# Kernel optimization log

Measured on AMD Instinct MI355X. Metric: run time of the kernel, lower is better.

The kernel has to match this reference:

```python
import jax, jax.numpy as jnp
import numpy as np
from jax import lax

L = 1024       # sequence length
D = 64         # bond_dim
O = 128        # output_dim
P = 2          # d_phys
B = 4096       # batch
SPLIT = L // 2


def _ident(dl, dr):
    # identity boost added to every physical slice: t[k, p, k] += 1 for k < min(dl, dr)
    m = min(dl, dr)
    base = jnp.zeros((dl, dr), dtype=jnp.float32)
    base = base.at[jnp.arange(m), jnp.arange(m)].set(1.0)
    return base[:, None, :]  # (dl, 1, dr) broadcast over p


def setup_inputs() -> dict:
    key = jax.random.key(0)
    k0, k1, k2, k3, k4, k5 = jax.random.split(key, 6)
    x = jax.random.uniform(k0, (B, L), dtype=jnp.float32)
    left0 = jax.random.normal(k1, (1, P, D), dtype=jnp.float32) * 0.01 + _ident(1, D)
    left_rest = jax.random.normal(k2, (SPLIT - 1, D, P, D), dtype=jnp.float32) * 0.01 + _ident(D, D)[None]
    center = jax.random.normal(k3, (D, D, O), dtype=jnp.float32) / jnp.sqrt(jnp.float32(O))
    right_rest = jax.random.normal(k4, (L - SPLIT - 1, D, P, D), dtype=jnp.float32) * 0.01 + _ident(D, D)[None]
    right_last = jax.random.normal(k5, (D, P, 1), dtype=jnp.float32) * 0.01 + _ident(D, 1)
    return {"x": x, "left0": left0, "left_rest": left_rest, "center": center,
            "right_rest": right_rest, "right_last": right_last}


def _norm_env(env):
    return env / (jnp.linalg.norm(env, axis=1, keepdims=True) + 1e-8)


def reference(x, left0, left_rest, center, right_rest, right_last):
    angle = (jnp.pi / 2.0) * x
    phi = jnp.stack([jnp.cos(angle), jnp.sin(angle)], axis=-1)  # (B, L, P)

    # left sweep: first tensor has trivial left bond (=1)
    left = _norm_env(jnp.einsum('pr,bp->br', left0[0], phi[:, 0]))

    def lstep(env, inp):
        A, p = inp  # A: (D,P,D), p: (B,P)
        return _norm_env(jnp.einsum('bl,lpr,bp->br', env, A, p)), None

    phi_l = jnp.swapaxes(phi[:, 1:SPLIT], 0, 1)  # (SPLIT-1, B, P)
    left, _ = lax.scan(lstep, left, (left_rest, phi_l))

    # right sweep (from last site inward): last tensor has trivial right bond (=1)
    right = _norm_env(jnp.einsum('lp,bp->bl', right_last[:, :, 0], phi[:, L - 1]))

    def rstep(env, inp):
        A, p = inp
        return _norm_env(jnp.einsum('br,lpr,bp->bl', env, A, p)), None

    phi_r = jnp.swapaxes(phi[:, SPLIT:L - 1], 0, 1)[::-1]  # reversed order
    right, _ = lax.scan(rstep, right, (right_rest[::-1], phi_r))

    out = jnp.einsum('bl,br,lro->bo', left, right, center)  # (B, O)
    # F.normalize(p=2, dim=1) with eps=1e-12
    return out / jnp.clip(jnp.linalg.norm(out, axis=1, keepdims=True), 1e-12)
```

## Files before the change

### kernel.cpp

```cpp
#include <hip/hip_runtime.h>

typedef float vf4 __attribute__((ext_vector_type(4)));
typedef int vi4 __attribute__((ext_vector_type(4)));
typedef short short8 __attribute__((ext_vector_type(8)));
typedef unsigned short ushort8 __attribute__((ext_vector_type(8)));

#define LL 1024
#define DD 64
#define OO 128
#define BBATCH 4096
#define NS 511
#define SITE_F 8192

__device__ __forceinline__ void gld_lds16(const float* g, float* l) {
  __builtin_amdgcn_global_load_lds(
      (const __attribute__((address_space(1))) unsigned int*)g,
      (__attribute__((address_space(3))) unsigned int*)l, 16, 0, 0);
}

__device__ __forceinline__ void stage32k_256(float* lds, const float* g, int tid) {
#pragma unroll
  for (int q = 0; q < 8; q++) {
    const int off = (q * 256 + tid) * 4;
    gld_lds16(g + off, lds + off);
  }
}

__global__ __launch_bounds__(256) void prep(const float* __restrict__ lsrc,
                                            const float* __restrict__ rsrc,
                                            unsigned short* __restrict__ Wl,
                                            unsigned short* __restrict__ Wr) {
  __shared__ float S[SITE_F];
  const int site = blockIdx.x;
  const int dir = blockIdx.y;
  const int tid = threadIdx.x;
  const float* src = (dir ? rsrc : lsrc) + (size_t)site * SITE_F;
  unsigned short* dst = dir ? (Wr + (size_t)(NS - 1 - site) * SITE_F)
                            : (Wl + (size_t)site * SITE_F);
#pragma unroll
  for (int m = 0; m < 8; m++)
    *(vf4*)&S[(m * 256 + tid) * 4] = *(const vf4*)&src[(m * 256 + tid) * 4];
  __syncthreads();
#pragma unroll
  for (int q = 0; q < 4; q++) {
    const int slot = q * 256 + tid;
    const int lane = slot & 63, f = slot >> 6;
    const int mt = f >> 2, s = f & 3;
    const int g = lane >> 4, c = lane & 15;
    const int m = 16 * mt + c;
    ushort8 t;
#pragma unroll
    for (int j = 0; j < 8; j++) {
      const int k = 32 * s + 8 * g + j;
      float v;
      if (dir == 0) {
        const int l = k >> 1, p = k & 1;
        v = S[l * 128 + p * 64 + m] - ((m == l) ? 1.f : 0.f);
      } else {
        const int r = k >> 1, p = k & 1;
        v = S[m * 128 + p * 64 + r] - ((m == r) ? 1.f : 0.f);
      }
      const unsigned uu = __builtin_bit_cast(unsigned, v);
      t[j] = (unsigned short)((uu + 0x7FFFu + ((uu >> 16) & 1u)) >> 16);
    }
    *(ushort8*)&dst[(size_t)slot * 8] = t;
  }
}

#define STAGE_GROUP(G, BUF)                                                    \
  {                                                                            \
    _Pragma("unroll")                                                          \
    for (int s4 = 0; s4 < 4; s4++) {                                           \
      int st_ = (G) * 4 + s4;                                                  \
      if (st_ > NS - 1) st_ = NS - 1;                                          \
      const float* Ws_ = Wf + (size_t)st_ * 4096;                              \
      float* d_ = &ring[BUF][s4][0];                                           \
      _Pragma("unroll")                                                        \
      for (int q = 0; q < 8; q++)                                              \
        gld_lds16(Ws_ + q * 512 + tid * 4, d_ + q * 512 + tid * 4);            \
    }                                                                          \
  }

#define BODY(I, BUF, S4)                                                       \
  {                                                                            \
    const float* rb = &ring[BUF][S4][0];                                       \
    vf4 FC[16];                                                                \
    _Pragma("unroll")                                                          \
    for (int q = 0; q < 16; q++)                                               \
      FC[q] = *(const vf4*)&rb[(q * 64 + lane) * 4];                           \
    const int nI = (I) + 1;                                                    \
    float xn = 0.f;                                                            \
    if (nI <= NS - 1) xn = xrow[dir ? (1022 - nI) : (1 + nI)];                 \
    short8 e2[4];                                                              \
    _Pragma("unroll")                                                          \
    for (int s = 0; s < 4; s++) {                                              \
      int pk[4];                                                               \
      _Pragma("unroll")                                                        \
      for (int t = 0; t < 4; t++) {                                            \
        const float f0 = u[s][t] * CS, f1 = u[s][t] * SN;                      \
        int p;                                                                 \
        asm("v_cvt_pk_bf16_f32 %0, %1, %2" : "=v"(p) : "v"(f0), "v"(f1));      \
        pk[t] = p;                                                             \
      }                                                                        \
      e2[s] = __builtin_bit_cast(short8, (vi4){pk[0], pk[1], pk[2], pk[3]});   \
    }                                                                          \
    const float keff = CS + SN;                                                \
    vf4 acc[4];                                                                \
    _Pragma("unroll")                                                          \
    for (int mt = 0; mt < 4; mt++) {                                           \
      vf4 z;                                                                   \
      z[0] = keff * u[mt][0]; z[1] = keff * u[mt][1];                          \
      z[2] = keff * u[mt][2]; z[3] = keff * u[mt][3];                          \
      acc[mt] = z;                                                             \
    }                                                                          \
    _Pragma("unroll")                                                          \
    for (int mt = 0; mt < 4; mt++) {                                           \
      acc[mt] = __builtin_amdgcn_mfma_f32_16x16x32_bf16(                       \
          __builtin_bit_cast(short8, FC[mt * 4 + 0]), e2[0], acc[mt], 0, 0, 0);\
      acc[mt] = __builtin_amdgcn_mfma_f32_16x16x32_bf16(                       \
          __builtin_bit_cast(short8, FC[mt * 4 + 1]), e2[1], acc[mt], 0, 0, 0);\
      acc[mt] = __builtin_amdgcn_mfma_f32_16x16x32_bf16(                       \
          __builtin_bit_cast(short8, FC[mt * 4 + 2]), e2[2], acc[mt], 0, 0, 0);\
      acc[mt] = __builtin_amdgcn_mfma_f32_16x16x32_bf16(                       \
          __builtin_bit_cast(short8, FC[mt * 4 + 3]), e2[3], acc[mt], 0, 0, 0);\
    }                                                                          \
    _Pragma("unroll")                                                          \
    for (int mt = 0; mt < 4; mt++) u[mt] = acc[mt];                            \
    if (nI <= NS - 1) {                                   \
      const float qrev = 0.25f * xn;           \
      float c_, s_;                                                            \
      asm("v_cos_f32 %0, %1" : "=v"(c_) : "v"(qrev));                          \
      asm("v_sin_f32 %0, %1" : "=v"(s_) : "v"(qrev));                          \
      CS = c_;                                                                 \
      SN = s_;                                                                 \
    }                                                                          \
    if (((I) & 7) == 7) {         \
      float nss = 0.f;                                                         \
      _Pragma("unroll")                                                        \
      for (int mt = 0; mt < 4; mt++)                                           \
        _Pragma("unroll")                                                      \
        for (int r = 0; r < 4; r++) nss += u[mt][r] * u[mt][r];                \
      nss += __shfl_xor(nss, 16);                                              \
      nss += __shfl_xor(nss, 32);                                              \
      const int eb = (__float_as_int(nss) >> 23) & 0xFF;                       \
      const float alpha = __int_as_float((127 - ((eb - 127) >> 1)) << 23);     \
      _Pragma("unroll")                                                        \
      for (int mt = 0; mt < 4; mt++)                                           \
        _Pragma("unroll")                                                      \
        for (int r = 0; r < 4; r++) u[mt][r] *= alpha;                         \
    }                                                                          \
  }

__global__ __launch_bounds__(128, 1) void sweep(const float* __restrict__ x,
                                                const float* __restrict__ left0,
                                                const float* __restrict__ right_last,
                                                const unsigned short* __restrict__ Wl,
                                                const unsigned short* __restrict__ Wr,
                                                float* __restrict__ envL,
                                                float* __restrict__ envR) {
  __shared__ float ring[2][4][4096];
  const int bid = blockIdx.x;
  const int xcd = bid & 7;
  const int dir = xcd >> 2;
  const int slot = (xcd & 3) * 32 + (bid >> 3);
  const int tid = threadIdx.x;
  const int wave = tid >> 6;
  const int lane = tid & 63;
  const int g_ = lane >> 4, c = lane & 15;
  const int b = (slot * 2 + wave) * 16 + c;
  const float* xrow = x + (size_t)b * LL;

  const float* Wf = (const float*)(dir ? Wr : Wl);

  vf4 u[4];
  {
    const float x0 = xrow[dir ? (LL - 1) : 0];
    const float qrev = 0.25f * x0;
    float cs, sn;
    asm("v_cos_f32 %0, %1" : "=v"(cs) : "v"(qrev));
    asm("v_sin_f32 %0, %1" : "=v"(sn) : "v"(qrev));
#pragma unroll
    for (int mt = 0; mt < 4; mt++)
#pragma unroll
      for (int r = 0; r < 4; r++) {
        const int n = 16 * mt + 4 * g_ + r;
        const float w0 = dir ? right_last[n * 2] : left0[n];
        const float w1 = dir ? right_last[n * 2 + 1] : left0[64 + n];
        u[mt][r] = cs * w0 + sn * w1;
      }
    float ss = 0.f;
#pragma unroll
    for (int mt = 0; mt < 4; mt++)
#pragma unroll
      for (int r = 0; r < 4; r++) ss += u[mt][r] * u[mt][r];
    ss += __shfl_xor(ss, 16);
    ss += __shfl_xor(ss, 32);
    const float a0 = 1.f / (sqrtf(ss) + 1e-8f);
#pragma unroll
    for (int mt = 0; mt < 4; mt++)
#pragma unroll
      for (int r = 0; r < 4; r++) u[mt][r] *= a0;
  }

  float CS, SN;
  {
    const float q0 = 0.25f * xrow[dir ? 1022 : 1];
    asm("v_cos_f32 %0, %1" : "=v"(CS) : "v"(q0));
    asm("v_sin_f32 %0, %1" : "=v"(SN) : "v"(q0));
  }

  STAGE_GROUP(0, 0)
  __syncthreads();

  for (int g = 0; g < 127; g++) {
    const int buf = g & 1;
    STAGE_GROUP(g + 1, buf ^ 1)
    const int i0 = g * 4;
    BODY(i0 + 0, buf, 0)
    BODY(i0 + 1, buf, 1)
    BODY(i0 + 2, buf, 2)
    BODY(i0 + 3, buf, 3)
    __syncthreads();
  }
  BODY(508, 1, 0)
  BODY(509, 1, 1)
  BODY(510, 1, 2)

  float nss = 0.f;
#pragma unroll
  for (int mt = 0; mt < 4; mt++)
#pragma unroll
    for (int r = 0; r < 4; r++) nss += u[mt][r] * u[mt][r];
  nss += __shfl_xor(nss, 16);
  nss += __shfl_xor(nss, 32);
  const float alpha = 1.f / (sqrtf(nss) + 1e-8f);

  float* eo = (dir ? envR : envL) + (size_t)b * 64;
#pragma unroll
  for (int mt = 0; mt < 4; mt++) {
    vf4 v;
#pragma unroll
    for (int r = 0; r < 4; r++) v[r] = u[mt][r] * alpha;
    *(vf4*)&eo[16 * mt + 4 * g_] = v;
  }
}

__global__ __launch_bounds__(256) void centerk(const float* __restrict__ envL,
                                               const float* __restrict__ envR,
                                               const float* __restrict__ center,
                                               float* __restrict__ Pp) {
  __shared__ float Cs[2][SITE_F];
  __shared__ float LT[64 * 36];
  __shared__ float RT[64 * 36];
  const int bbase = blockIdx.x * 32;
  const int half = blockIdx.y;
  const int tid = threadIdx.x;
  const int och = tid & 31, bch = tid >> 5;
  const int o0 = och * 4, b0 = bch * 4;
#pragma unroll
  for (int m = 0; m < 8; m++) {
    const int idx = m * 256 + tid;
    const int b = idx >> 6, l = idx & 63;
    LT[l * 36 + b] = envL[(bbase + b) * 64 + l];
    RT[l * 36 + b] = envR[(bbase + b) * 64 + l];
  }
  stage32k_256(Cs[0], center + (half * 32) * SITE_F, tid);
  float acc[4][4] = {};
  for (int lh = 0; lh < 32; lh++) {
    __syncthreads();
    const int buf = lh & 1;
    if (lh + 1 < 32) stage32k_256(Cs[buf ^ 1], center + (half * 32 + lh + 1) * SITE_F, tid);
    const vf4 lv = *(const vf4*)&LT[(half * 32 + lh) * 36 + b0];
    const float* C = Cs[buf];
#pragma unroll
    for (int r = 0; r < 64; r++) {
      const vf4 rv = *(const vf4*)&RT[r * 36 + b0];
      const vf4 cv = *(const vf4*)&C[r * 128 + o0];
#pragma unroll
      for (int i2 = 0; i2 < 4; i2++) {
        const float w = lv[i2] * rv[i2];
        acc[i2][0] += w * cv[0];
        acc[i2][1] += w * cv[1];
        acc[i2][2] += w * cv[2];
        acc[i2][3] += w * cv[3];
      }
    }
  }
#pragma unroll
  for (int i2 = 0; i2 < 4; i2++) {
    vf4 v; v[0] = acc[i2][0]; v[1] = acc[i2][1]; v[2] = acc[i2][2]; v[3] = acc[i2][3];
    *(vf4*)&Pp[(size_t)half * BBATCH * 128 + (size_t)(bbase + b0 + i2) * 128 + o0] = v;
  }
}

__global__ __launch_bounds__(256) void combinek(const float* __restrict__ P,
                                                float* __restrict__ out) {
  const float* P0 = P;
  const float* P1 = P + (size_t)BBATCH * 128;
  const int row = blockIdx.x * 8 + (threadIdx.x >> 5);
  const int o0 = (threadIdx.x & 31) * 4;
  vf4 v = *(const vf4*)&P0[(size_t)row * 128 + o0];
  const vf4 v1 = *(const vf4*)&P1[(size_t)row * 128 + o0];
  v += v1;
  float ss = v[0] * v[0] + v[1] * v[1] + v[2] * v[2] + v[3] * v[3];
#pragma unroll
  for (int m = 1; m < 32; m <<= 1) ss += __shfl_xor(ss, m);
  const float inv = 1.f / fmaxf(sqrtf(ss), 1e-12f);
  v *= inv;
  *(vf4*)&out[(size_t)row * 128 + o0] = v;
}

extern "C" void kernel_launch(void* const* d_in, const int* in_sizes, int n_in,
                              void* d_out, int out_size, void* d_ws, size_t ws_size,
                              hipStream_t stream) {
  const float* x = (const float*)d_in[0];
  const float* left0 = (const float*)d_in[1];
  const float* left_rest = (const float*)d_in[2];
  const float* center = (const float*)d_in[3];
  const float* right_rest = (const float*)d_in[4];
  const float* right_last = (const float*)d_in[5];
  float* out = (float*)d_out;

  char* wsb = (char*)d_ws;
  unsigned short* Wl = (unsigned short*)wsb;
  unsigned short* Wr = Wl + (size_t)NS * SITE_F;
  float* envL = (float*)(Wr + (size_t)NS * SITE_F);
  float* envR = envL + (size_t)BBATCH * 64;
  float* Pp = envR + (size_t)BBATCH * 64;

  hipLaunchKernelGGL(prep, dim3(NS, 2), dim3(256), 0, stream,
                     left_rest, right_rest, Wl, Wr);
  hipLaunchKernelGGL(sweep, dim3(256), dim3(128), 0, stream,
                     x, left0, right_last, Wl, Wr, envL, envR);
  hipLaunchKernelGGL(centerk, dim3(BBATCH / 32, 2), dim3(256), 0, stream,
                     envL, envR, center, Pp);
  hipLaunchKernelGGL(combinek, dim3(BBATCH / 8), dim3(256), 0, stream, Pp, out);
}
```

Before: 387.6 us.

## Use bf16 MFMA for center contraction and prefetch sweep fragments across sites

The center contraction now runs on bf16 MFMA instead of scalar FP32 FMAs. A new prep2 kernel reformats the center tensor into MFMA fragment layout, and the sweep also writes a bf16 copy of the right environment. Separately, the sweep loop loads the next site's LDS fragments into registers before the current MFMAs run, and splits each accumulation chain into two independent accumulators to shorten dependency latency. The center output no longer needs the two-half partial sum, which simplifies the combine step. In exchange it adds a kernel launch, raises register pressure in the sweep, and lowers precision in the center product.

```diff
diff --git a/kernel.cpp b/kernel.cpp
--- a/kernel.cpp
+++ b/kernel.cpp
@@ -2,6 +2,7 @@
 
 typedef float vf4 __attribute__((ext_vector_type(4)));
 typedef int vi4 __attribute__((ext_vector_type(4)));
+typedef int vi2 __attribute__((ext_vector_type(2)));
 typedef short short8 __attribute__((ext_vector_type(8)));
 typedef unsigned short ushort8 __attribute__((ext_vector_type(8)));
 
@@ -18,12 +19,9 @@
       (__attribute__((address_space(3))) unsigned int*)l, 16, 0, 0);
 }
 
-__device__ __forceinline__ void stage32k_256(float* lds, const float* g, int tid) {
-#pragma unroll
-  for (int q = 0; q < 8; q++) {
-    const int off = (q * 256 + tid) * 4;
-    gld_lds16(g + off, lds + off);
-  }
+__device__ __forceinline__ unsigned short f2bf(float v) {
+  const unsigned uu = __builtin_bit_cast(unsigned, v);
+  return (unsigned short)((uu + 0x7FFFu + ((uu >> 16) & 1u)) >> 16);
 }
 
 __global__ __launch_bounds__(256) void prep(const float* __restrict__ lsrc,
@@ -60,10 +58,37 @@
         const int r = k >> 1, p = k & 1;
         v = S[m * 128 + p * 64 + r] - ((m == r) ? 1.f : 0.f);
       }
-      const unsigned uu = __builtin_bit_cast(unsigned, v);
-      t[j] = (unsigned short)((uu + 0x7FFFu + ((uu >> 16) & 1u)) >> 16);
+      t[j] = f2bf(v);
     }
     *(ushort8*)&dst[(size_t)slot * 8] = t;
+  }
+}
+
+__global__ __launch_bounds__(256) void prep2(const float* __restrict__ center,
+                                             unsigned short* __restrict__ Cf) {
+  __shared__ float S[4096];
+  const int o = blockIdx.x;
+  const int tid = threadIdx.x;
+#pragma unroll
+  for (int k = 0; k < 16; k++) {
+    const int idx = k * 256 + tid;
+    S[idx] = center[(size_t)idx * 128 + o];
+  }
+  __syncthreads();
+#pragma unroll
+  for (int q = 0; q < 2; q++) {
+    const int slot = q * 256 + tid;
+    const int lane = slot & 63, f = slot >> 6;
+    const int mt = f >> 1, s = f & 1;
+    const int g = lane >> 4, c = lane & 15;
+    const int l = 16 * mt + c;
+    ushort8 t;
+#pragma unroll
+    for (int j = 0; j < 8; j++) {
+      const int r = 32 * s + 8 * g + j;
+      t[j] = f2bf(S[l * 64 + r]);
+    }
+    *(ushort8*)&Cf[(size_t)((o * 8 + f) * 64 + lane) * 8] = t;
   }
 }
 
@@ -81,13 +106,20 @@
     }                                                                          \
   }
 
-#define BODY(I, BUF, S4)                                                       \
+#define LOAD_FC(FC, RB)                                                        \
   {                                                                            \
-    const float* rb = &ring[BUF][S4][0];                                       \
-    vf4 FC[16];                                                                \
+    const float* rb_ = (RB);                                                   \
     _Pragma("unroll")                                                          \
     for (int q = 0; q < 16; q++)                                               \
-      FC[q] = *(const vf4*)&rb[(q * 64 + lane) * 4];                           \
+      FC[q] = *(const vf4*)&rb_[(q * 64 + lane) * 4];                          \
+  }
+
+#define BODYP(I, FCc, FCn, RBN, PF)                                            \
+  {                                                                            \
+    if (PF) {                                                                  \
+      LOAD_FC(FCn, RBN)                                                        \
+      __builtin_amdgcn_sched_barrier(0);                                       \
+    }                                                                          \
     const int nI = (I) + 1;                                                    \
     float xn = 0.f;                                                            \
     if (nI <= NS - 1) xn = xrow[dir ? (1022 - nI) : (1 + nI)];                 \
@@ -105,28 +137,29 @@
       e2[s] = __builtin_bit_cast(short8, (vi4){pk[0], pk[1], pk[2], pk[3]});   \
     }                                                                          \
     const float keff = CS + SN;                                                \
-    vf4 acc[4];                                                                \
+    vf4 accA[4], accB[4];                                                      \
     _Pragma("unroll")                                                          \
     for (int mt = 0; mt < 4; mt++) {                                           \
       vf4 z;                                                                   \
       z[0] = keff * u[mt][0]; z[1] = keff * u[mt][1];                          \
       z[2] = keff * u[mt][2]; z[3] = keff * u[mt][3];                          \
-      acc[mt] = z;                                                             \
+      accA[mt] = z;                                                            \
+      accB[mt] = (vf4){0.f, 0.f, 0.f, 0.f};                                    \
     }                                                                          \
     _Pragma("unroll")                                                          \
     for (int mt = 0; mt < 4; mt++) {                                           \
-      acc[mt] = __builtin_amdgcn_mfma_f32_16x16x32_bf16(                       \
-          __builtin_bit_cast(short8, FC[mt * 4 + 0]), e2[0], acc[mt], 0, 0, 0);\
-      acc[mt] = __builtin_amdgcn_mfma_f32_16x16x32_bf16(                       \
-          __builtin_bit_cast(short8, FC[mt * 4 + 1]), e2[1], acc[mt], 0, 0, 0);\
-      acc[mt] = __builtin_amdgcn_mfma_f32_16x16x32_bf16(                       \
-          __builtin_bit_cast(short8, FC[mt * 4 + 2]), e2[2], acc[mt], 0, 0, 0);\
-      acc[mt] = __builtin_amdgcn_mfma_f32_16x16x32_bf16(                       \
-          __builtin_bit_cast(short8, FC[mt * 4 + 3]), e2[3], acc[mt], 0, 0, 0);\
-    }                                                                          \
-    _Pragma("unroll")                                                          \
-    for (int mt = 0; mt < 4; mt++) u[mt] = acc[mt];                            \
-    if (nI <= NS - 1) {                                   \
+      accA[mt] = __builtin_amdgcn_mfma_f32_16x16x32_bf16(                      \
+          __builtin_bit_cast(short8, FCc[mt * 4 + 0]), e2[0], accA[mt], 0,0,0);\
+      accA[mt] = __builtin_amdgcn_mfma_f32_16x16x32_bf16(                      \
+          __builtin_bit_cast(short8, FCc[mt * 4 + 1]), e2[1], accA[mt], 0,0,0);\
+      accB[mt] = __builtin_amdgcn_mfma_f32_16x16x32_bf16(                      \
+          __builtin_bit_cast(short8, FCc[mt * 4 + 2]), e2[2], accB[mt], 0,0,0);\
+      accB[mt] = __builtin_amdgcn_mfma_f32_16x16x32_bf16(                      \
+          __builtin_bit_cast(short8, FCc[mt * 4 + 3]), e2[3], accB[mt], 0,0,0);\
+    }                                                                          \
+    _Pragma("unroll")                                                          \
+    for (int mt = 0; mt < 4; mt++) u[mt] = accA[mt] + accB[mt];                \
+    if (nI <= NS - 1) {                                                        \
       const float qrev = 0.25f * xn;           \
       float c_, s_;                                                            \
       asm("v_cos_f32 %0, %1" : "=v"(c_) : "v"(qrev));                          \
@@ -134,7 +167,7 @@
       CS = c_;                                                                 \
       SN = s_;                                                                 \
     }                                                                          \
-    if (((I) & 7) == 7) {         \
+    if (((I) & 7) == 7) {                              \
       float nss = 0.f;                                                         \
       _Pragma("unroll")                                                        \
       for (int mt = 0; mt < 4; mt++)                                           \
@@ -157,7 +190,9 @@
                                                 const unsigned short* __restrict__ Wl,
                                                 const unsigned short* __restrict__ Wr,
                                                 float* __restrict__ envL,
-                                                float* __restrict__ envR) {
+                                                float* __restrict__ envR,
+                                                unsigned short* __restrict__ Lb16,
+                                                unsigned short* __restrict__ Rb16) {
   __shared__ float ring[2][4][4096];
   const int bid = blockIdx.x;
   const int xcd = bid & 7;
@@ -212,19 +247,22 @@
   STAGE_GROUP(0, 0)
   __syncthreads();
 
+  vf4 fX[16], fY[16];
   for (int g = 0; g < 127; g++) {
     const int buf = g & 1;
+    LOAD_FC(fX, &ring[buf][0][0])
     STAGE_GROUP(g + 1, buf ^ 1)
     const int i0 = g * 4;
-    BODY(i0 + 0, buf, 0)
-    BODY(i0 + 1, buf, 1)
-    BODY(i0 + 2, buf, 2)
-    BODY(i0 + 3, buf, 3)
+    BODYP(i0 + 0, fX, fY, &ring[buf][1][0], 1)
+    BODYP(i0 + 1, fY, fX, &ring[buf][2][0], 1)
+    BODYP(i0 + 2, fX, fY, &ring[buf][3][0], 1)
+    BODYP(i0 + 3, fY, fX, &ring[buf][0][0], 0)
     __syncthreads();
   }
-  BODY(508, 1, 0)
-  BODY(509, 1, 1)
-  BODY(510, 1, 2)
+  LOAD_FC(fX, &ring[1][0][0])
+  BODYP(508, fX, fY, &ring[1][1][0], 1)
+  BODYP(509, fY, fX, &ring[1][2][0], 1)
+  BODYP(510, fX, fY, &ring[1][3][0], 0)
 
   float nss = 0.f;
 #pragma unroll
@@ -236,72 +274,72 @@
   const float alpha = 1.f / (sqrtf(nss) + 1e-8f);
 
   float* eo = (dir ? envR : envL) + (size_t)b * 64;
+  unsigned short* eo16 = (dir ? Rb16 : Lb16) + (size_t)b * 64;
 #pragma unroll
   for (int mt = 0; mt < 4; mt++) {
     vf4 v;
 #pragma unroll
     for (int r = 0; r < 4; r++) v[r] = u[mt][r] * alpha;
     *(vf4*)&eo[16 * mt + 4 * g_] = v;
-  }
-}
-
-__global__ __launch_bounds__(256) void centerk(const float* __restrict__ envL,
-                                               const float* __restrict__ envR,
-                                               const float* __restrict__ center,
-                                               float* __restrict__ Pp) {
-  __shared__ float Cs[2][SITE_F];
-  __shared__ float LT[64 * 36];
-  __shared__ float RT[64 * 36];
-  const int bbase = blockIdx.x * 32;
-  const int half = blockIdx.y;
+    int p01, p23;
+    asm("v_cvt_pk_bf16_f32 %0, %1, %2" : "=v"(p01) : "v"(v[0]), "v"(v[1]));
+    asm("v_cvt_pk_bf16_f32 %0, %1, %2" : "=v"(p23) : "v"(v[2]), "v"(v[3]));
+    *(vi2*)&eo16[16 * mt + 4 * g_] = (vi2){p01, p23};
+  }
+}
+
+__global__ __launch_bounds__(256) void centerk2(const float* __restrict__ envL,
+                                                const unsigned short* __restrict__ Rb16,
+                                                const unsigned short* __restrict__ Cf,
+                                                float* __restrict__ Pp) {
+  const int b0 = blockIdx.x * 16;
   const int tid = threadIdx.x;
-  const int och = tid & 31, bch = tid >> 5;
-  const int o0 = och * 4, b0 = bch * 4;
-#pragma unroll
-  for (int m = 0; m < 8; m++) {
-    const int idx = m * 256 + tid;
-    const int b = idx >> 6, l = idx & 63;
-    LT[l * 36 + b] = envL[(bbase + b) * 64 + l];
-    RT[l * 36 + b] = envR[(bbase + b) * 64 + l];
-  }
-  stage32k_256(Cs[0], center + (half * 32) * SITE_F, tid);
-  float acc[4][4] = {};
-  for (int lh = 0; lh < 32; lh++) {
-    __syncthreads();
-    const int buf = lh & 1;
-    if (lh + 1 < 32) stage32k_256(Cs[buf ^ 1], center + (half * 32 + lh + 1) * SITE_F, tid);
-    const vf4 lv = *(const vf4*)&LT[(half * 32 + lh) * 36 + b0];
-    const float* C = Cs[buf];
-#pragma unroll
-    for (int r = 0; r < 64; r++) {
-      const vf4 rv = *(const vf4*)&RT[r * 36 + b0];
-      const vf4 cv = *(const vf4*)&C[r * 128 + o0];
-#pragma unroll
-      for (int i2 = 0; i2 < 4; i2++) {
-        const float w = lv[i2] * rv[i2];
-        acc[i2][0] += w * cv[0];
-        acc[i2][1] += w * cv[1];
-        acc[i2][2] += w * cv[2];
-        acc[i2][3] += w * cv[3];
-      }
+  const int wave = tid >> 6;
+  const int lane = tid & 63;
+  const int g = lane >> 4, c = lane & 15;
+
+  short8 rf[2];
+#pragma unroll
+  for (int s = 0; s < 2; s++)
+    rf[s] = __builtin_bit_cast(short8,
+        *(const ushort8*)&Rb16[(size_t)(b0 + c) * 64 + 32 * s + 8 * g]);
+
+  vf4 Lv[4];
+#pragma unroll
+  for (int mt = 0; mt < 4; mt++)
+    Lv[mt] = *(const vf4*)&envL[(size_t)(b0 + c) * 64 + 16 * mt + 4 * g];
+
+  for (int oi = 0; oi < 32; oi++) {
+    const int o = wave * 32 + oi;
+    const unsigned short* cb = Cf + (size_t)(o * 8) * 64 * 8;
+    vf4 acc[4];
+#pragma unroll
+    for (int mt = 0; mt < 4; mt++) {
+      const short8 a0 = __builtin_bit_cast(short8,
+          *(const ushort8*)&cb[(size_t)((mt * 2 + 0) * 64 + lane) * 8]);
+      const short8 a1 = __builtin_bit_cast(short8,
+          *(const ushort8*)&cb[(size_t)((mt * 2 + 1) * 64 + lane) * 8]);
+      vf4 z = {0.f, 0.f, 0.f, 0.f};
+      z = __builtin_amdgcn_mfma_f32_16x16x32_bf16(a0, rf[0], z, 0, 0, 0);
+      z = __builtin_amdgcn_mfma_f32_16x16x32_bf16(a1, rf[1], z, 0, 0, 0);
+      acc[mt] = z;
     }
-  }
-#pragma unroll
-  for (int i2 = 0; i2 < 4; i2++) {
-    vf4 v; v[0] = acc[i2][0]; v[1] = acc[i2][1]; v[2] = acc[i2][2]; v[3] = acc[i2][3];
-    *(vf4*)&Pp[(size_t)half * BBATCH * 128 + (size_t)(bbase + b0 + i2) * 128 + o0] = v;
-  }
-}
-
-__global__ __launch_bounds__(256) void combinek(const float* __restrict__ P,
-                                                float* __restrict__ out) {
-  const float* P0 = P;
-  const float* P1 = P + (size_t)BBATCH * 128;
+    float ps = 0.f;
+#pragma unroll
+    for (int mt = 0; mt < 4; mt++)
+#pragma unroll
+      for (int r = 0; r < 4; r++) ps += Lv[mt][r] * acc[mt][r];
+    ps += __shfl_xor(ps, 16);
+    ps += __shfl_xor(ps, 32);
+    if (g == 0) Pp[(size_t)(b0 + c) * 128 + o] = ps;
+  }
+}
+
+__global__ __launch_bounds__(256) void combinek2(const float* __restrict__ P,
+                                                 float* __restrict__ out) {
   const int row = blockIdx.x * 8 + (threadIdx.x >> 5);
   const int o0 = (threadIdx.x & 31) * 4;
-  vf4 v = *(const vf4*)&P0[(size_t)row * 128 + o0];
-  const vf4 v1 = *(const vf4*)&P1[(size_t)row * 128 + o0];
-  v += v1;
+  vf4 v = *(const vf4*)&P[(size_t)row * 128 + o0];
   float ss = v[0] * v[0] + v[1] * v[1] + v[2] * v[2] + v[3] * v[3];
 #pragma unroll
   for (int m = 1; m < 32; m <<= 1) ss += __shfl_xor(ss, m);
@@ -326,13 +364,17 @@
   unsigned short* Wr = Wl + (size_t)NS * SITE_F;
   float* envL = (float*)(Wr + (size_t)NS * SITE_F);
   float* envR = envL + (size_t)BBATCH * 64;
-  float* Pp = envR + (size_t)BBATCH * 64;
+  unsigned short* Lb16 = (unsigned short*)(envR + (size_t)BBATCH * 64);
+  unsigned short* Rb16 = Lb16 + (size_t)BBATCH * 64;
+  unsigned short* Cf = Rb16 + (size_t)BBATCH * 64;
+  float* Pp = (float*)(Cf + (size_t)OO * 8 * 64 * 8);
 
   hipLaunchKernelGGL(prep, dim3(NS, 2), dim3(256), 0, stream,
                      left_rest, right_rest, Wl, Wr);
+  hipLaunchKernelGGL(prep2, dim3(OO), dim3(256), 0, stream, center, Cf);
   hipLaunchKernelGGL(sweep, dim3(256), dim3(128), 0, stream,
-                     x, left0, right_last, Wl, Wr, envL, envR);
-  hipLaunchKernelGGL(centerk, dim3(BBATCH / 32, 2), dim3(256), 0, stream,
-                     envL, envR, center, Pp);
-  hipLaunchKernelGGL(combinek, dim3(BBATCH / 8), dim3(256), 0, stream, Pp, out);
-}
+                     x, left0, right_last, Wl, Wr, envL, envR, Lb16, Rb16);
+  hipLaunchKernelGGL(centerk2, dim3(BBATCH / 16), dim3(256), 0, stream,
+                     envL, Rb16, Cf, Pp);
+  hipLaunchKernelGGL(combinek2, dim3(BBATCH / 8), dim3(256), 0, stream, Pp, out);
+}
```

Measured after the change: 320.2 us. 17.4% less time.
